# Kernel optimization log

Hardware: AMD Instinct MI355X
Metric: run time of the kernel (lower is better)

## Reference

```python
import jax, jax.numpy as jnp
import numpy as np

# static multi-scale pyramid (must match spatial_shapes array in setup_inputs)
SPATIAL = ((100, 100), (50, 50), (25, 25), (13, 13))
E, H, L, P = 256, 8, 4, 8   # embed_dims, num_heads, num_levels, num_points
BS, NQ = 2, 10000
LEN_VAL = sum(h * w for h, w in SPATIAL)


def _bilinear_gather(val, grid, Hs, Ws):
    """val: [BH, Hs*Ws, d]; grid: [BH, N, 2] in [-1,1].
    Matches F.grid_sample(mode='bilinear', padding_mode='zeros', align_corners=False)."""
    x = (grid[..., 0] + 1.0) * (Ws * 0.5) - 0.5
    y = (grid[..., 1] + 1.0) * (Hs * 0.5) - 0.5
    x0 = jnp.floor(x).astype(jnp.int32)
    y0 = jnp.floor(y).astype(jnp.int32)
    x1, y1 = x0 + 1, y0 + 1
    wx1 = x - x0.astype(x.dtype)
    wy1 = y - y0.astype(y.dtype)
    wx0, wy0 = 1.0 - wx1, 1.0 - wy1

    def corner(xi, yi, w):
        valid = (xi >= 0) & (xi < Ws) & (yi >= 0) & (yi < Hs)
        idx = jnp.clip(yi, 0, Hs - 1) * Ws + jnp.clip(xi, 0, Ws - 1)  # [BH, N]
        v = jnp.take_along_axis(val, idx[..., None], axis=1)          # [BH, N, d]
        return v * (w * valid.astype(w.dtype))[..., None]

    return (corner(x0, y0, wx0 * wy0) + corner(x1, y0, wx1 * wy0)
            + corner(x0, y1, wx0 * wy1) + corner(x1, y1, wx1 * wy1))


def setup_inputs() -> dict:
    key = jax.random.key(0)
    ks = jax.random.split(key, 10)
    scale = 1.0 / np.sqrt(E)
    inp = {
        'query': jax.random.normal(ks[0], (BS, NQ, E), jnp.float32),
        'value': jax.random.normal(ks[1], (BS, LEN_VAL, E), jnp.float32),
        'query_pos': 0.1 * jax.random.normal(ks[2], (BS, NQ, E), jnp.float32),
        'reference_points': jax.random.uniform(ks[3], (BS, NQ, L, 2), jnp.float32),
        'spatial_shapes': jnp.array(SPATIAL, dtype=jnp.int32),
        'W_off': 0.02 * jax.random.normal(ks[4], (E, H * L * P * 2), jnp.float32),
        'b_off': 0.5 * jax.random.normal(ks[5], (H * L * P * 2,), jnp.float32),
        'W_attn': 0.02 * jax.random.normal(ks[6], (E, H * L * P), jnp.float32),
        'b_attn': jnp.zeros((H * L * P,), jnp.float32),
        'W_val': scale * jax.random.normal(ks[7], (E, E), jnp.float32),
        'b_val': jnp.zeros((E,), jnp.float32),
        'W_out': scale * jax.random.normal(ks[8], (E, E), jnp.float32),
        'b_out': jnp.zeros((E,), jnp.float32),
    }
    return inp


def reference(query, value, query_pos, reference_points, spatial_shapes,
              W_off, b_off, W_attn, b_attn, W_val, b_val, W_out, b_out):
    d = E // H
    q = query + query_pos                                        # [bs, nq, E]
    bs, nq, _ = q.shape
    v = (value @ W_val + b_val).reshape(bs, LEN_VAL, H, d)       # [bs, len, H, d]
    off = (q @ W_off + b_off).reshape(bs, nq, H, L, P, 2)
    aw = jax.nn.softmax((q @ W_attn + b_attn).reshape(bs, nq, H, L * P), axis=-1)
    aw = aw.reshape(bs, nq, H, L, P)
    # normalizer is (W, H) per level
    norm = jnp.stack([spatial_shapes[:, 1], spatial_shapes[:, 0]], -1).astype(q.dtype)
    loc = reference_points[:, :, None, :, None, :] + off / norm[None, None, None, :, None, :]
    grids = 2.0 * loc - 1.0                                      # [bs, nq, H, L, P, 2]

    out = jnp.zeros((bs, nq, H, d), q.dtype)
    start = 0
    for lvl, (Hs, Ws) in enumerate(SPATIAL):
        v_l = v[:, start:start + Hs * Ws]                        # [bs, HW, H, d]
        start += Hs * Ws
        v_l = v_l.transpose(0, 2, 1, 3).reshape(bs * H, Hs * Ws, d)
        g_l = grids[:, :, :, lvl].transpose(0, 2, 1, 3, 4).reshape(bs * H, nq * P, 2)
        s = _bilinear_gather(v_l, g_l, Hs, Ws).reshape(bs, H, nq, P, d)
        w_l = aw[:, :, :, lvl].transpose(0, 2, 1, 3)             # [bs, H, nq, P]
        out = out + jnp.einsum('bhnpc,bhnp->bnhc', s, w_l)
    return out.reshape(bs, nq, E) @ W_out + b_out
```

## Files before the change

### kernel.cpp

```cpp
#include <hip/hip_runtime.h>


#define EE   256
#define HH   8
#define LL   4
#define NQq  10000
#define BSB  2
#define LENV 13294
#define MQ   16
#define ROWS_V (BSB * LENV)

typedef unsigned short u16;
typedef unsigned int   u32;
typedef __attribute__((ext_vector_type(8))) short bf16x8;
typedef __attribute__((ext_vector_type(4))) float f32x4;

__device__ __forceinline__ u32 bf16_of(float f) {
  u32 u = __float_as_uint(f);
  return (u + 0x7FFFu + ((u >> 16) & 1u)) >> 16;
}
__device__ __forceinline__ float bf2f(u32 u) { return __uint_as_float(u << 16); }

__device__ __forceinline__ uint4 pack8(const float* f) {
  uint4 u;
  u.x = bf16_of(f[0]) | (bf16_of(f[1]) << 16);
  u.y = bf16_of(f[2]) | (bf16_of(f[3]) << 16);
  u.z = bf16_of(f[4]) | (bf16_of(f[5]) << 16);
  u.w = bf16_of(f[6]) | (bf16_of(f[7]) << 16);
  return u;
}

__global__ __launch_bounds__(64) void k_prep(
    const float* __restrict__ W_off, const float* __restrict__ W_attn,
    const float* __restrict__ W_val, const float* __restrict__ W_out,
    u16* __restrict__ wcat, u16* __restrict__ wval, u16* __restrict__ wout) {
  const int tile = blockIdx.x >> 3, s = blockIdx.x & 7;
  const int l = threadIdx.x, quad = l >> 4, r16 = l & 15;
  float f[8];
  u16* dst;
  if (tile < 48) {
    int col = tile * 16 + r16;
#pragma unroll
    for (int j = 0; j < 8; ++j) {
      int k = s * 32 + quad * 8 + j;
      f[j] = (col < 512) ? W_off[k * 512 + col] : W_attn[k * 256 + (col - 512)];
    }
    dst = wcat + ((tile * 8 + s) * 64 + l) * 8;
  } else if (tile < 64) {
    int col = (tile - 48) * 16 + r16;
#pragma unroll
    for (int j = 0; j < 8; ++j) f[j] = W_val[(s * 32 + quad * 8 + j) * 256 + col];
    dst = wval + (((tile - 48) * 8 + s) * 64 + l) * 8;
  } else {
    int col = (tile - 64) * 16 + r16;
#pragma unroll
    for (int j = 0; j < 8; ++j) f[j] = W_out[(s * 32 + quad * 8 + j) * 256 + col];
    dst = wout + (((tile - 64) * 8 + s) * 64 + l) * 8;
  }
  *(uint4*)dst = pack8(f);
}

__global__ __launch_bounds__(256) void k_valproj(
    const float* __restrict__ value, const float* __restrict__ b_val,
    const u16* __restrict__ wval, u16* __restrict__ v_ws) {
  __shared__ __align__(16) u16 sA[64][264];
  const int tid = threadIdx.x;
  const int g0 = blockIdx.x * 64;
#pragma unroll
  for (int ch = 0; ch < 8; ++ch) {
    int fidx = ch * 2048 + tid * 8;
    int row = fidx >> 8, col = fidx & 255;
    int g = g0 + row;
    float fv[8] = {0.f, 0.f, 0.f, 0.f, 0.f, 0.f, 0.f, 0.f};
    if (g < ROWS_V) {
      float4 a = *(const float4*)(value + (long)g * 256 + col);
      float4 b = *(const float4*)(value + (long)g * 256 + col + 4);
      fv[0] = a.x; fv[1] = a.y; fv[2] = a.z; fv[3] = a.w;
      fv[4] = b.x; fv[5] = b.y; fv[6] = b.z; fv[7] = b.w;
    }
    *(uint4*)&sA[row][col] = pack8(fv);
  }
  __syncthreads();
  const int wave = tid >> 6, lane = tid & 63, quad = lane >> 4, r16 = lane & 15;
  f32x4 acc[4][4] = {};
  for (int s = 0; s < 8; ++s) {
    bf16x8 af[4];
#pragma unroll
    for (int mt = 0; mt < 4; ++mt)
      af[mt] = *(const bf16x8*)&sA[mt * 16 + r16][s * 32 + quad * 8];
#pragma unroll
    for (int nt = 0; nt < 4; ++nt) {
      bf16x8 bfg = *(const bf16x8*)(wval + (((wave * 4 + nt) * 8 + s) * 64 + lane) * 8);
#pragma unroll
      for (int mt = 0; mt < 4; ++mt)
        acc[nt][mt] = __builtin_amdgcn_mfma_f32_16x16x32_bf16(af[mt], bfg, acc[nt][mt], 0, 0, 0);
    }
  }
  __syncthreads();
#pragma unroll
  for (int nt = 0; nt < 4; ++nt) {
    int col = (wave * 4 + nt) * 16 + r16;
    float bias = b_val[col];
#pragma unroll
    for (int mt = 0; mt < 4; ++mt)
#pragma unroll
      for (int rr = 0; rr < 4; ++rr)
        sA[mt * 16 + quad * 4 + rr][col] = (u16)bf16_of(acc[nt][mt][rr] + bias);
  }
  __syncthreads();
  const int h = tid >> 5, c = tid & 31;
  for (int r = 0; r < 64; ++r) {
    int g = g0 + r;
    if (g >= ROWS_V) break;
    int b = g / LENV, pix = g - b * LENV;
    v_ws[((b * 8 + h) * LENV + pix) * 32 + c] = sA[r][tid];
  }
}

__global__ __launch_bounds__(512, 4) void k_attn(
    const float* __restrict__ query, const float* __restrict__ query_pos,
    const float* __restrict__ refpts,
    const float* __restrict__ b_off, const float* __restrict__ b_attn,
    const float* __restrict__ b_out,
    const u16* __restrict__ wcat, const u16* __restrict__ wout,
    const u16* __restrict__ v_ws, float* __restrict__ out) {
  __shared__ __align__(16) char smem[65536];
  u16   (*sQ)[264]  = (u16(*)[264])smem;
  float (*sC)[772]  = (float(*)[772])smem;
  uint4 (*sTab)[256] = (uint4(*)[256])smem;
  u16   (*sO)[264]  = (u16(*)[264])smem;

  const int tid = threadIdx.x;
  const int g0 = blockIdx.x * MQ;
  const int b = g0 / NQq;
  const int q0 = g0 - b * NQq;
  const int wave = tid >> 6, lane = tid & 63, quad = lane >> 4, r16 = lane & 15;

  {
    int fidx = tid * 8;
    int row = fidx >> 8, col = fidx & 255;
    long base = ((long)(b * NQq + q0 + row)) * 256 + col;
    float4 a0 = *(const float4*)(query + base);
    float4 a1 = *(const float4*)(query + base + 4);
    float4 p0 = *(const float4*)(query_pos + base);
    float4 p1 = *(const float4*)(query_pos + base + 4);
    float fv[8] = {a0.x + p0.x, a0.y + p0.y, a0.z + p0.z, a0.w + p0.w,
                   a1.x + p1.x, a1.y + p1.y, a1.z + p1.z, a1.w + p1.w};
    *(uint4*)&sQ[row][col] = pack8(fv);
  }
  __syncthreads();

  f32x4 acc[6] = {};
  for (int s = 0; s < 8; ++s) {
    bf16x8 af = *(const bf16x8*)&sQ[r16][s * 32 + quad * 8];
#pragma unroll
    for (int t6 = 0; t6 < 6; ++t6) {
      int tile = wave * 6 + t6;
      bf16x8 bfg = *(const bf16x8*)(wcat + ((tile * 8 + s) * 64 + lane) * 8);
      acc[t6] = __builtin_amdgcn_mfma_f32_16x16x32_bf16(af, bfg, acc[t6], 0, 0, 0);
    }
  }
  __syncthreads();
#pragma unroll
  for (int t6 = 0; t6 < 6; ++t6) {
    int col = (wave * 6 + t6) * 16 + r16;
#pragma unroll
    for (int rr = 0; rr < 4; ++rr)
      sC[quad * 4 + rr][col] = acc[t6][rr];
  }
  __syncthreads();

  if (tid < MQ * HH) {
    int m = tid >> 3, h = tid & 7;
    float* p = &sC[m][512 + h * 32];
    const float* ba = b_attn + h * 32;
    float mx = -1e30f;
    for (int j = 0; j < 32; ++j) { float v = p[j] + ba[j]; p[j] = v; mx = fmaxf(mx, v); }
    float sum = 0.f;
    for (int j = 0; j < 32; ++j) { float e = __expf(p[j] - mx); p[j] = e; sum += e; }
    float inv = 1.f / sum;
    for (int j = 0; j < 32; ++j) p[j] *= inv;
  }
  __syncthreads();

  uint4 recs[8];
  {
    const int s = tid & 255, mh = tid >> 8;
    const int l = (s >> 3) & 3;
    const int WlI[4] = {100, 50, 25, 13};
    const int baseI[4] = {0, 10000, 12500, 13125};
    const int Wl = WlI[l], Hl = WlI[l], base = baseI[l];
    const float WlF = (float)Wl;
    const float box = b_off[2 * s], boy = b_off[2 * s + 1];
#pragma unroll
    for (int mm = 0; mm < 8; ++mm) {
      int m = mh * 8 + mm;
      float w = sC[m][512 + s];
      float ax = sC[m][2 * s], ay = sC[m][2 * s + 1];
      float2 rp = *(const float2*)(refpts + (((long)(b * NQq + q0 + m)) * LL + l) * 2);
      float x = rp.x * WlF + (ax + box) - 0.5f;
      float y = rp.y * WlF + (ay + boy) - 0.5f;
      float fx0 = floorf(x), fy0 = floorf(y);
      int x0 = (int)fx0, y0 = (int)fy0;
      float fx = x - fx0, fy = y - fy0;
      bool xv0 = (x0 >= 0) & (x0 < Wl);
      bool xv1 = (x0 >= -1) & (x0 < Wl - 1);
      bool yv0 = (y0 >= 0) & (y0 < Hl);
      bool yv1 = (y0 >= -1) & (y0 < Hl - 1);
      float w00 = w * (1.f - fx) * (1.f - fy) * (float)(xv0 & yv0);
      float w01 = w * fx * (1.f - fy) * (float)(xv1 & yv0);
      float w10 = w * (1.f - fx) * fy * (float)(xv0 & yv1);
      float w11 = w * fx * fy * (float)(xv1 & yv1);
      int x0c = min(max(x0, 0), Wl - 1);
      int x1c = min(max(x0 + 1, 0), Wl - 1);
      int y0c = min(max(y0, 0), Hl - 1);
      int y1c = min(max(y0 + 1, 0), Hl - 1);
      u32 o00 = (u32)(base + y0c * Wl + x0c) * 32u;
      u32 dx = (u32)(x1c - x0c) * 32u;
      u32 dy = (u32)(y1c - y0c) * (u32)Wl * 32u;
      uint4 rec;
      rec.x = bf16_of(w00) | (bf16_of(w01) << 16);
      rec.y = bf16_of(w10) | (bf16_of(w11) << 16);
      rec.z = o00;
      rec.w = (dx << 16) | dy;
      recs[mm] = rec;
    }
  }
  __syncthreads();
  {
    const int s = tid & 255, mh = tid >> 8;
#pragma unroll
    for (int mm = 0; mm < 8; ++mm) sTab[mh * 8 + mm][s] = recs[mm];
  }
  __syncthreads();

  const int half = tid >> 8, h = (tid >> 5) & 7, c = tid & 31;
  float oacc[8] = {};
  {
    const u32 hcb = ((u32)(b * 8 + h) * (u32)LENV) * 32u + (u32)c;
    for (int i = 0; i < 32; ++i) {
      int srow = h * 32 + i;
#pragma unroll
      for (int mm = 0; mm < 8; ++mm) {
        uint4 r = sTab[half * 8 + mm][srow];
        float w00 = __uint_as_float(r.x << 16);
        float w01 = __uint_as_float(r.x & 0xFFFF0000u);
        float w10 = __uint_as_float(r.y << 16);
        float w11 = __uint_as_float(r.y & 0xFFFF0000u);
        u32 dx = r.w >> 16, dy = r.w & 0xFFFFu;
        u32 o00 = hcb + r.z;
        float v00 = bf2f((u32)v_ws[o00]);
        float v01 = bf2f((u32)v_ws[o00 + dx]);
        float v10 = bf2f((u32)v_ws[o00 + dy]);
        float v11 = bf2f((u32)v_ws[o00 + dx + dy]);
        oacc[mm] += w00 * v00 + w01 * v01 + w10 * v10 + w11 * v11;
      }
    }
  }
  __syncthreads();
#pragma unroll
  for (int mm = 0; mm < 8; ++mm)
    sO[half * 8 + mm][h * 32 + c] = (u16)bf16_of(oacc[mm]);
  __syncthreads();

  f32x4 acc2[2] = {};
  for (int s = 0; s < 8; ++s) {
    bf16x8 af = *(const bf16x8*)&sO[r16][s * 32 + quad * 8];
#pragma unroll
    for (int t2 = 0; t2 < 2; ++t2) {
      int tile = wave * 2 + t2;
      bf16x8 bfg = *(const bf16x8*)(wout + ((tile * 8 + s) * 64 + lane) * 8);
      acc2[t2] = __builtin_amdgcn_mfma_f32_16x16x32_bf16(af, bfg, acc2[t2], 0, 0, 0);
    }
  }
#pragma unroll
  for (int t2 = 0; t2 < 2; ++t2) {
    int col = (wave * 2 + t2) * 16 + r16;
    float bias = b_out[col];
#pragma unroll
    for (int rr = 0; rr < 4; ++rr) {
      int row = quad * 4 + rr;
      out[((long)(b * NQq + q0 + row)) * 256 + col] = acc2[t2][rr] + bias;
    }
  }
}

extern "C" void kernel_launch(void* const* d_in, const int* in_sizes, int n_in,
                              void* d_out, int out_size, void* d_ws, size_t ws_size,
                              hipStream_t stream) {
  const float* query     = (const float*)d_in[0];
  const float* value     = (const float*)d_in[1];
  const float* query_pos = (const float*)d_in[2];
  const float* refpts    = (const float*)d_in[3];
  const float* W_off     = (const float*)d_in[5];
  const float* b_off     = (const float*)d_in[6];
  const float* W_attn    = (const float*)d_in[7];
  const float* b_attn    = (const float*)d_in[8];
  const float* W_val     = (const float*)d_in[9];
  const float* b_val     = (const float*)d_in[10];
  const float* W_out     = (const float*)d_in[11];
  const float* b_out     = (const float*)d_in[12];
  float* out = (float*)d_out;

  char* ws = (char*)d_ws;
  u16* v_ws = (u16*)ws;
  u16* wcat = (u16*)(ws + 13613056);
  u16* wval = (u16*)(ws + 13613056 + 393216);
  u16* wout = (u16*)(ws + 13613056 + 393216 + 131072);

  k_prep<<<dim3(80 * 8), dim3(64), 0, stream>>>(W_off, W_attn, W_val, W_out,
                                                wcat, wval, wout);
  k_valproj<<<dim3((ROWS_V + 63) / 64), dim3(256), 0, stream>>>(value, b_val, wval, v_ws);
  k_attn<<<dim3(BSB * NQq / MQ), dim3(512), 0, stream>>>(
      query, query_pos, refpts, b_off, b_attn, b_out, wcat, wout, v_ws, out);
}
```

Baseline: 269.3 us.

## Vectorize bilinear gather to 16-byte loads with per-thread 8-channel ownership

Each thread in the sampling loop now owns eight channels of one query-head pair and fetches each bilinear corner as one 16-byte load, replacing scalar 2-byte gathers. Corner offsets use a clamp to -1 so the x+1 neighbour is a fixed +64 byte step. The sampling table is swizzled to avoid LDS bank conflicts. The value-projection store becomes 16-byte vectorized writes and the softmax is spread over all threads with shuffles. A clamp to -1 can read one row before the buffer, and that read only gets weight zero, so the value workspace is moved to sit after the weight block to keep such reads in bounds.

```diff
diff --git a/kernel.cpp b/kernel.cpp
--- a/kernel.cpp
+++ b/kernel.cpp
@@ -10,6 +10,8 @@
 #define MQ   16
 #define ROWS_V (BSB * LENV)
 
+#define VWS_OFF 393216
+
 typedef unsigned short u16;
 typedef unsigned int   u32;
 typedef __attribute__((ext_vector_type(8))) short bf16x8;
@@ -19,7 +21,8 @@
   u32 u = __float_as_uint(f);
   return (u + 0x7FFFu + ((u >> 16) & 1u)) >> 16;
 }
-__device__ __forceinline__ float bf2f(u32 u) { return __uint_as_float(u << 16); }
+__device__ __forceinline__ float blo(u32 u) { return __uint_as_float(u << 16); }
+__device__ __forceinline__ float bhi(u32 u) { return __uint_as_float(u & 0xFFFF0000u); }
 
 __device__ __forceinline__ uint4 pack8(const float* f) {
   uint4 u;
@@ -28,6 +31,13 @@
   u.z = bf16_of(f[4]) | (bf16_of(f[5]) << 16);
   u.w = bf16_of(f[6]) | (bf16_of(f[7]) << 16);
   return u;
+}
+
+__device__ __forceinline__ void acc8(float o[8], uint4 q, float w) {
+  o[0] += w * blo(q.x); o[1] += w * bhi(q.x);
+  o[2] += w * blo(q.y); o[3] += w * bhi(q.y);
+  o[4] += w * blo(q.z); o[5] += w * bhi(q.z);
+  o[6] += w * blo(q.w); o[7] += w * bhi(q.w);
 }
 
 __global__ __launch_bounds__(64) void k_prep(
@@ -108,12 +118,18 @@
         sA[mt * 16 + quad * 4 + rr][col] = (u16)bf16_of(acc[nt][mt][rr] + bias);
   }
   __syncthreads();
-  const int h = tid >> 5, c = tid & 31;
-  for (int r = 0; r < 64; ++r) {
+#pragma unroll
+  for (int it = 0; it < 8; ++it) {
+    int chunk = it * 256 + tid;
+    int r  = chunk >> 5;
+    int hc = chunk & 31;
+    int h2 = hc >> 2, qq = hc & 3;
     int g = g0 + r;
-    if (g >= ROWS_V) break;
-    int b = g / LENV, pix = g - b * LENV;
-    v_ws[((b * 8 + h) * LENV + pix) * 32 + c] = sA[r][tid];
+    if (g < ROWS_V) {
+      int bb = g / LENV, pix = g - bb * LENV;
+      *(uint4*)(v_ws + ((long)((bb * 8 + h2) * LENV + pix) * 32 + qq * 8)) =
+          *(const uint4*)&sA[r][h2 * 32 + qq * 8];
+    }
   }
 }
 
@@ -123,7 +139,7 @@
     const float* __restrict__ b_off, const float* __restrict__ b_attn,
     const float* __restrict__ b_out,
     const u16* __restrict__ wcat, const u16* __restrict__ wout,
-    const u16* __restrict__ v_ws, float* __restrict__ out) {
+    const char* __restrict__ wsb, float* __restrict__ out) {
   __shared__ __align__(16) char smem[65536];
   u16   (*sQ)[264]  = (u16(*)[264])smem;
   float (*sC)[772]  = (float(*)[772])smem;
@@ -170,16 +186,24 @@
   }
   __syncthreads();
 
-  if (tid < MQ * HH) {
-    int m = tid >> 3, h = tid & 7;
-    float* p = &sC[m][512 + h * 32];
-    const float* ba = b_attn + h * 32;
+  {
+    const int m = tid >> 5, hh = (tid >> 2) & 7, g = tid & 3;
+    float* p = &sC[m][512 + hh * 32 + g * 8];
+    const float* ba = b_attn + hh * 32 + g * 8;
+    float v[8];
     float mx = -1e30f;
-    for (int j = 0; j < 32; ++j) { float v = p[j] + ba[j]; p[j] = v; mx = fmaxf(mx, v); }
+#pragma unroll
+    for (int j = 0; j < 8; ++j) { v[j] = p[j] + ba[j]; mx = fmaxf(mx, v[j]); }
+    mx = fmaxf(mx, __shfl_xor(mx, 1));
+    mx = fmaxf(mx, __shfl_xor(mx, 2));
     float sum = 0.f;
-    for (int j = 0; j < 32; ++j) { float e = __expf(p[j] - mx); p[j] = e; sum += e; }
+#pragma unroll
+    for (int j = 0; j < 8; ++j) { v[j] = __expf(v[j] - mx); sum += v[j]; }
+    sum += __shfl_xor(sum, 1);
+    sum += __shfl_xor(sum, 2);
     float inv = 1.f / sum;
-    for (int j = 0; j < 32; ++j) p[j] *= inv;
+#pragma unroll
+    for (int j = 0; j < 8; ++j) p[j] = v[j] * inv;
   }
   __syncthreads();
 
@@ -211,56 +235,52 @@
       float w01 = w * fx * (1.f - fy) * (float)(xv1 & yv0);
       float w10 = w * (1.f - fx) * fy * (float)(xv0 & yv1);
       float w11 = w * fx * fy * (float)(xv1 & yv1);
-      int x0c = min(max(x0, 0), Wl - 1);
-      int x1c = min(max(x0 + 1, 0), Wl - 1);
-      int y0c = min(max(y0, 0), Hl - 1);
+      int x0a = min(max(x0, -1), Wl - 1);
+      int y0a = min(max(y0, -1), Hl - 1);
       int y1c = min(max(y0 + 1, 0), Hl - 1);
-      u32 o00 = (u32)(base + y0c * Wl + x0c) * 32u;
-      u32 dx = (u32)(x1c - x0c) * 32u;
-      u32 dy = (u32)(y1c - y0c) * (u32)Wl * 32u;
+      int o00 = (base + y0a * Wl + x0a) * 64;
+      u32 dyb = (u32)((y1c - y0a) * Wl) * 64u;
       uint4 rec;
       rec.x = bf16_of(w00) | (bf16_of(w01) << 16);
       rec.y = bf16_of(w10) | (bf16_of(w11) << 16);
-      rec.z = o00;
-      rec.w = (dx << 16) | dy;
+      rec.z = (u32)o00;
+      rec.w = dyb;
       recs[mm] = rec;
     }
   }
   __syncthreads();
   {
     const int s = tid & 255, mh = tid >> 8;
-#pragma unroll
-    for (int mm = 0; mm < 8; ++mm) sTab[mh * 8 + mm][s] = recs[mm];
-  }
-  __syncthreads();
-
-  const int half = tid >> 8, h = (tid >> 5) & 7, c = tid & 31;
-  float oacc[8] = {};
-  {
-    const u32 hcb = ((u32)(b * 8 + h) * (u32)LENV) * 32u + (u32)c;
+    const int jsw = (s & 224) | ((s + (s >> 5)) & 31);
+#pragma unroll
+    for (int mm = 0; mm < 8; ++mm) sTab[mh * 8 + mm][jsw] = recs[mm];
+  }
+  __syncthreads();
+
+  {
+    const int c4 = tid & 3, hh = (tid >> 2) & 7, m = tid >> 5;
+    const u32 vb = (u32)VWS_OFF + (u32)(b * 8 + hh) * (u32)(LENV * 64) + (u32)c4 * 16u;
+    float oacc[8] = {};
+#pragma unroll 4
     for (int i = 0; i < 32; ++i) {
-      int srow = h * 32 + i;
-#pragma unroll
-      for (int mm = 0; mm < 8; ++mm) {
-        uint4 r = sTab[half * 8 + mm][srow];
-        float w00 = __uint_as_float(r.x << 16);
-        float w01 = __uint_as_float(r.x & 0xFFFF0000u);
-        float w10 = __uint_as_float(r.y << 16);
-        float w11 = __uint_as_float(r.y & 0xFFFF0000u);
-        u32 dx = r.w >> 16, dy = r.w & 0xFFFFu;
-        u32 o00 = hcb + r.z;
-        float v00 = bf2f((u32)v_ws[o00]);
-        float v01 = bf2f((u32)v_ws[o00 + dx]);
-        float v10 = bf2f((u32)v_ws[o00 + dy]);
-        float v11 = bf2f((u32)v_ws[o00 + dx + dy]);
-        oacc[mm] += w00 * v00 + w01 * v01 + w10 * v10 + w11 * v11;
-      }
-    }
-  }
-  __syncthreads();
-#pragma unroll
-  for (int mm = 0; mm < 8; ++mm)
-    sO[half * 8 + mm][h * 32 + c] = (u16)bf16_of(oacc[mm]);
+      const int srow = (hh << 5) | ((i + hh) & 31);
+      uint4 r = sTab[m][srow];
+      u32 off0 = vb + r.z;
+      u32 off1 = off0 + r.w;
+      uint4 q00 = *(const uint4*)(wsb + off0);
+      uint4 q01 = *(const uint4*)(wsb + off0 + 64);
+      uint4 q10 = *(const uint4*)(wsb + off1);
+      uint4 q11 = *(const uint4*)(wsb + off1 + 64);
+      float w00 = blo(r.x), w01 = bhi(r.x);
+      float w10 = blo(r.y), w11 = bhi(r.y);
+      acc8(oacc, q00, w00);
+      acc8(oacc, q01, w01);
+      acc8(oacc, q10, w10);
+      acc8(oacc, q11, w11);
+    }
+    __syncthreads();
+    *(uint4*)&sO[m][hh * 32 + c4 * 8] = pack8(oacc);
+  }
   __syncthreads();
 
   f32x4 acc2[2] = {};
@@ -303,14 +323,14 @@
   float* out = (float*)d_out;
 
   char* ws = (char*)d_ws;
-  u16* v_ws = (u16*)ws;
-  u16* wcat = (u16*)(ws + 13613056);
-  u16* wval = (u16*)(ws + 13613056 + 393216);
-  u16* wout = (u16*)(ws + 13613056 + 393216 + 131072);
+  u16* wcat = (u16*)ws;
+  u16* v_ws = (u16*)(ws + VWS_OFF);
+  u16* wval = (u16*)(ws + VWS_OFF + 13613056);
+  u16* wout = (u16*)(ws + VWS_OFF + 13613056 + 131072);
 
   k_prep<<<dim3(80 * 8), dim3(64), 0, stream>>>(W_off, W_attn, W_val, W_out,
                                                 wcat, wval, wout);
   k_valproj<<<dim3((ROWS_V + 63) / 64), dim3(256), 0, stream>>>(value, b_val, wval, v_ws);
   k_attn<<<dim3(BSB * NQq / MQ), dim3(512), 0, stream>>>(
-      query, query_pos, refpts, b_off, b_attn, b_out, wcat, wout, v_ws, out);
-}
+      query, query_pos, refpts, b_off, b_attn, b_out, wcat, wout, ws, out);
+}
```

New measurement: 244.0 us. 9.4% less time.
